# Optimization experiments

Hardware: AMD Instinct MI355X
Metric: run time of the kernel (lower is better)

The kernel has to match this reference:

```python
import jax, jax.numpy as jnp
import numpy as np

EPS = 1.1920929e-07  # torch.finfo(float32).eps, default for F.rms_norm


def _rms_norm(x):
    # F.rms_norm(x, (D,)) with no weight
    return x * jax.lax.rsqrt(jnp.mean(jnp.square(x), axis=-1, keepdims=True) + EPS)


def setup_inputs() -> dict:
    key = jax.random.key(0)
    ks = jax.random.split(key, 10)
    B, T, V, C, NB = 4, 4096, 512, 512, 64
    s = 0.02
    return {
        "x": jax.random.normal(ks[0], (B, T, V), dtype=jnp.float32),
        "basis": jax.random.normal(ks[1], (V, 2 * NB), dtype=jnp.float32),
        # AssociativeMemoryStep params
        "q_coeffs": jax.random.normal(ks[2], (C, 2 * NB), dtype=jnp.float32) * s,
        "k_coeffs": jax.random.normal(ks[3], (C, 2 * NB), dtype=jnp.float32) * s,
        "v_coeffs": jax.random.normal(ks[4], (C, 2 * NB), dtype=jnp.float32) * s,
        "o_coeffs": jax.random.normal(ks[5], (C, 2 * NB), dtype=jnp.float32) * s,
        "decay_logit": jnp.float32(3.0),
        "mem_out_scale": jnp.float32(0.1),
        # FourierRegisterOp params
        "read_coeffs": jax.random.normal(ks[6], (C, 2 * NB), dtype=jnp.float32) * s,
        "write_coeffs": jax.random.normal(ks[7], (C, 2 * NB), dtype=jnp.float32) * s,
        "channel_mix": jax.random.normal(ks[8], (C, C), dtype=jnp.float32) * s,
        "bias": jnp.zeros((C,), dtype=jnp.float32),
        "op_out_scale": jnp.float32(0.1),
        # RegisterStep scales
        "mem_scale": jnp.ones((1,), dtype=jnp.float32),
        "op_scale": jnp.ones((1,), dtype=jnp.float32),
    }


def reference(x, basis, q_coeffs, k_coeffs, v_coeffs, o_coeffs, decay_logit,
              mem_out_scale, read_coeffs, write_coeffs, channel_mix, bias,
              op_out_scale, mem_scale, op_scale):
    B, T, V = x.shape
    dt = x.dtype

    # ---- AssociativeMemoryStep on rms_norm(x) ----
    xn = _rms_norm(x)
    q_w = basis @ q_coeffs.T  # [V, C]
    k_w = basis @ k_coeffs.T
    v_w = basis @ v_coeffs.T
    o_w = basis @ o_coeffs.T
    q = xn @ q_w  # [B, T, C]
    k = xn @ k_w
    v = xn @ v_w
    scores = jnp.einsum('btc,bsc->bts', q, k)  # [B, T, T]
    decay = jax.nn.sigmoid(decay_logit)
    pos = jnp.arange(T)
    diff = pos[None, :] - pos[:, None]  # diff[t, s] = s - t
    expn = jnp.maximum(diff - 1, 0).astype(dt)
    decay_w = jnp.power(decay.astype(dt), expn) * (diff > 0).astype(dt)  # [T, T]
    retrieved = jnp.einsum('bts,bsc->btc', scores * decay_w[None], v)
    mem_out = (retrieved @ o_w.T) * mem_out_scale.astype(dt)  # [B, T, V]
    x = x + mem_scale.astype(dt) * mem_out

    # ---- FourierRegisterOp on rms_norm(x) ----
    xn2 = _rms_norm(x)
    read_w = jax.nn.softmax(basis @ read_coeffs.T, axis=0).astype(dt)  # [V, C]
    vals = xn2 @ read_w @ channel_mix.astype(dt) + bias.astype(dt)  # [B, T, C]
    vals = jax.nn.gelu(vals, approximate=False)  # torch F.gelu default = exact
    write_w = (basis @ write_coeffs.T).astype(dt)  # [V, C]
    op_out = (vals @ write_w.T) * op_out_scale.astype(dt)  # [B, T, V]
    return x + op_scale.astype(dt) * op_out
```

## Files before the change

kernel.cpp:

```cpp
#include <hip/hip_runtime.h>
#include <math.h>

typedef __attribute__((ext_vector_type(8))) short bvec8;
typedef __attribute__((ext_vector_type(4))) short bvec4;
typedef __attribute__((ext_vector_type(4))) float fvec4;
typedef unsigned short u16;

#define MROWS 16384
#define TLEN  4096
#define DD    512
#define SWB   256
#define NT128 32
#define EPS_RMS 1.1920929e-07f

#define M_SCORE  1
#define M_RETRES 2
#define M_RSGELU 3
#define M_BRES   4

__device__ __forceinline__ u16 f2bf(float f) {
  unsigned int u = __float_as_uint(f);
  u = (u + 0x7fffu + ((u >> 16) & 1u)) >> 16;
  return (u16)u;
}
__device__ __forceinline__ float bf2f(u16 u) {
  return __uint_as_float(((unsigned int)u) << 16);
}

__device__ __forceinline__ float wred_sum(float v) {
#pragma unroll
  for (int off = 32; off > 0; off >>= 1) v += __shfl_xor(v, off, 64);
  return v;
}
__device__ __forceinline__ float wred_max(float v) {
#pragma unroll
  for (int off = 32; off > 0; off >>= 1) v = fmaxf(v, __shfl_xor(v, off, 64));
  return v;
}

__device__ __forceinline__ int xcd_swz(int bid, int chunk) {
  return (bid & 7) * chunk + (bid >> 3);
}

#define GL16(g, l) __builtin_amdgcn_global_load_lds((const __attribute__((address_space(1))) unsigned int*)(g), (__attribute__((address_space(3))) unsigned int*)(l), 16, 0, 0)

__device__ __forceinline__ void gcore(
    const u16* __restrict__ Ab, int lda,
    const u16* __restrict__ Bb, int ldb,
    u16* lds, int NT, fvec4 (*acc)[4])
{
  const int tid = threadIdx.x, lane = tid & 63, w = tid >> 6;
  const int r = lane & 15, kg = lane >> 4;
  const int wn = (w & 1) * 64;
  const int ahalf = w >> 1;
  const int ar = tid >> 3, as = (tid & 7) ^ (ar & 7);
  const int br = tid >> 2, bs = (tid & 3) ^ (br & 3);
  const u16* a0r0 = Ab + (size_t)ar * lda + as * 8;
  const u16* a0r1 = a0r0 + (size_t)32 * lda;
  const u16* a1r0 = a0r0 + (size_t)64 * lda;
  const u16* a1r1 = a0r0 + (size_t)96 * lda;
  const u16* b0r0 = Bb + (size_t)br * ldb + bs * 8;
  const u16* b0r1 = b0r0 + (size_t)64 * ldb;
  u16* ldsw = lds + w * 512;

  bvec8 af[2], bfr[4];
#define ST_A0(kt,p) { GL16(a0r0+(kt)*64, ldsw+(p)*16384+0);     GL16(a0r1+(kt)*64, ldsw+(p)*16384+2048); }
#define ST_A1(kt,p) { GL16(a1r0+(kt)*64, ldsw+(p)*16384+4096);  GL16(a1r1+(kt)*64, ldsw+(p)*16384+6144); }
#define ST_B0(kt,p) { GL16(b0r0+(kt)*64, ldsw+(p)*16384+8192);  GL16(b0r1+(kt)*64, ldsw+(p)*16384+10240); }
#define ST_B1(kt,p) { GL16(b0r0+(kt)*64+32, ldsw+(p)*16384+12288); GL16(b0r1+(kt)*64+32, ldsw+(p)*16384+14336); }
#define RD_A(mq,ks,p) { const u16* Ac = lds + (p)*16384 + ahalf*4096; \
  af[0] = *(const bvec8*)&Ac[((((mq)*2+0)*16+r)*64) + ((((ks)*4+kg)^(r&7)))*8]; \
  af[1] = *(const bvec8*)&Ac[((((mq)*2+1)*16+r)*64) + ((((ks)*4+kg)^(r&7)))*8]; }
#define RD_B(ks,p) { const u16* Bc = lds + (p)*16384 + 8192 + (ks)*4096; \
  _Pragma("unroll") for (int ni=0;ni<4;++ni) bfr[ni] = *(const bvec8*)&Bc[((wn+ni*16+r)*32) + ((kg^(r&3)))*8]; }
#define MM(mq) { __builtin_amdgcn_s_setprio(1); \
  _Pragma("unroll") for (int i=0;i<2;++i) _Pragma("unroll") for (int ni=0;ni<4;++ni) \
  acc[(mq)*2+i][ni] = __builtin_amdgcn_mfma_f32_16x16x32_bf16(af[i], bfr[ni], acc[(mq)*2+i][ni], 0,0,0); \
  __builtin_amdgcn_s_setprio(0); }

  ST_A0(0,0); ST_A1(0,0); ST_B0(0,0); ST_B1(0,0);
  ST_B0(1,1);
  asm volatile("s_waitcnt vmcnt(2)" ::: "memory");
  __builtin_amdgcn_s_barrier();
  asm volatile("" ::: "memory");
  int cur = 0;
  for (int j = 0; j < NT - 1; ++j) {
    int nx = cur ^ 1, kt = j + 1;
    ST_B1(kt,nx); ST_A0(kt,nx); ST_A1(kt,nx);
    RD_A(0,0,cur); RD_B(0,cur); MM(0);
    RD_A(1,0,cur); MM(1);
    asm volatile("s_waitcnt lgkmcnt(0)" ::: "memory");
    __builtin_amdgcn_s_barrier();
    asm volatile("" ::: "memory");
    if (j + 2 < NT) { ST_B0(j+2,cur); }
    RD_A(0,1,cur); RD_B(1,cur); MM(0);
    RD_A(1,1,cur); MM(1);
    if (j + 2 < NT) {
      asm volatile("s_waitcnt vmcnt(2) lgkmcnt(0)" ::: "memory");
    } else {
      asm volatile("s_waitcnt vmcnt(0) lgkmcnt(0)" ::: "memory");
    }
    __builtin_amdgcn_s_barrier();
    asm volatile("" ::: "memory");
    cur = nx;
  }
  RD_A(0,0,cur); RD_B(0,cur); MM(0);
  RD_A(1,0,cur); MM(1);
  RD_A(0,1,cur); RD_B(1,cur); MM(0);
  RD_A(1,1,cur); MM(1);
#undef ST_A0
#undef ST_A1
#undef ST_B0
#undef ST_B1
#undef RD_A
#undef RD_B
#undef MM
}

__global__ __launch_bounds__(256, 2) void qkv256_kernel(
    const u16* __restrict__ xb, const u16* __restrict__ qkw,
    const u16* __restrict__ wvoT,
    u16* __restrict__ qb, u16* __restrict__ kb, u16* __restrict__ voT)
{
  __shared__ __align__(16) u16 As[8192];
  __shared__ __align__(16) u16 Bs[16384];
  int tid = threadIdx.x, lane = tid & 63, w = tid >> 6;
  int r = lane & 15, kg = lane >> 4;
  int wm = (w >> 1) * 64, wn = (w & 1) * 128;

  int nb = xcd_swz(blockIdx.x, 96);
  const u16 *Ab, *Bb;
  size_t om, on;
  int vmode = 0;
  if (nb < 512) {
    Ab = xb + (size_t)(nb >> 2) * 128 * 512;
    Bb = qkw + (size_t)(nb & 3) * 256 * 512;
    om = (size_t)(nb >> 2) * 128; on = (size_t)(nb & 3) * 256;
  } else {
    vmode = 1;
    int i = nb - 512;
    Ab = wvoT + (size_t)(i >> 6) * 128 * 512;
    Bb = xb + (size_t)(i & 63) * 256 * 512;
    om = (size_t)(i >> 6) * 128; on = (size_t)(i & 63) * 256;
  }

  const u16* ap = Ab + (size_t)(tid >> 3) * 512 + (((tid & 7) ^ ((tid >> 3) & 7)) * 8);
  const u16* bp = Bb + (size_t)(tid >> 3) * 512 + (((tid & 7) ^ ((tid >> 3) & 7)) * 8);

  fvec4 acc[4][8] = {};
  for (int kt = 0; kt < 8; ++kt) {
    __builtin_amdgcn_s_barrier();
    asm volatile("" ::: "memory");
#pragma unroll
    for (int l = 0; l < 4; ++l)
      GL16(ap + (size_t)(32 * l) * 512 + kt * 64, As + w * 512 + l * 2048);
#pragma unroll
    for (int l = 0; l < 8; ++l)
      GL16(bp + (size_t)(32 * l) * 512 + kt * 64, Bs + w * 512 + l * 2048);
    asm volatile("s_waitcnt vmcnt(0)" ::: "memory");
    __builtin_amdgcn_s_barrier();
    asm volatile("" ::: "memory");
    bvec8 af[4], bf[8];
#pragma unroll
    for (int ks = 0; ks < 2; ++ks) {
#pragma unroll
      for (int mi = 0; mi < 4; ++mi) {
        int rw = wm + mi * 16 + r;
        af[mi] = *(const bvec8*)&As[rw * 64 + ((ks * 4 + kg) ^ (rw & 7)) * 8];
      }
#pragma unroll
      for (int ni = 0; ni < 8; ++ni) {
        int rw = wn + ni * 16 + r;
        bf[ni] = *(const bvec8*)&Bs[rw * 64 + ((ks * 4 + kg) ^ (rw & 7)) * 8];
      }
      __builtin_amdgcn_s_setprio(1);
#pragma unroll
      for (int mi = 0; mi < 4; ++mi)
#pragma unroll
        for (int ni = 0; ni < 8; ++ni)
          acc[mi][ni] = __builtin_amdgcn_mfma_f32_16x16x32_bf16(af[mi], bf[ni], acc[mi][ni], 0, 0, 0);
      __builtin_amdgcn_s_setprio(0);
    }
  }

  int l15 = lane & 15, lr4 = (lane >> 4) << 2;
#pragma unroll
  for (int mi = 0; mi < 4; ++mi)
#pragma unroll
    for (int ni = 0; ni < 8; ++ni)
#pragma unroll
      for (int j = 0; j < 4; ++j) {
        size_t rr = om + wm + mi * 16 + lr4 + j;
        size_t c = on + wn + ni * 16 + l15;
        float v = acc[mi][ni][j];
        if (vmode == 0) {
          u16* o = (c < 512) ? qb : kb;
          o[rr * 512 + (c & 511)] = f2bf(v);
        } else {
          voT[rr * (size_t)MROWS + c] = f2bf(v);
        }
      }
}

__global__ __launch_bounds__(256) void conv7_kernel(
    const float* __restrict__ basis, const float* __restrict__ qc, const float* __restrict__ kc,
    const float* __restrict__ vc, const float* __restrict__ oc, const float* __restrict__ rc,
    const float* __restrict__ wc,
    u16* __restrict__ basisb, u16* __restrict__ qcb, u16* __restrict__ kcb,
    u16* __restrict__ vcb, u16* __restrict__ ocb, u16* __restrict__ rcb,
    u16* __restrict__ wcb)
{
  const float* src; u16* dst;
  switch (blockIdx.y) {
    case 0: src = basis; dst = basisb; break;
    case 1: src = qc; dst = qcb; break;
    case 2: src = kc; dst = kcb; break;
    case 3: src = vc; dst = vcb; break;
    case 4: src = oc; dst = ocb; break;
    case 5: src = rc; dst = rcb; break;
    default: src = wc; dst = wcb; break;
  }
  int idx = blockIdx.x * 256 + threadIdx.x;
  float4 v = ((const float4*)src)[idx];
  union { bvec4 s; u16 u[4]; } o;
  o.u[0] = f2bf(v.x); o.u[1] = f2bf(v.y); o.u[2] = f2bf(v.z); o.u[3] = f2bf(v.w);
  ((bvec4*)dst)[idx] = o.s;
}

__global__ __launch_bounds__(256, 2) void wgen_kernel(
    const u16* __restrict__ basisb, const u16* __restrict__ qcb,
    const u16* __restrict__ kcb, const u16* __restrict__ vcb,
    const u16* __restrict__ ocb, const u16* __restrict__ wcb,
    const u16* __restrict__ rcb,
    u16* __restrict__ qwT, u16* __restrict__ kwT,
    u16* __restrict__ vwB, u16* __restrict__ owB,
    u16* __restrict__ wrB, float* __restrict__ readLog)
{
  __shared__ __align__(16) u16 lds[32768];
  int tid = threadIdx.x, lane = tid & 63, wave = tid >> 6;
  int wm = (wave >> 1) * 64, wn = (wave & 1) * 64;
  int z = blockIdx.z;
  const u16 *Az, *Bz;
  switch (z) {
    case 0: Az = qcb;    Bz = basisb; break;
    case 1: Az = kcb;    Bz = basisb; break;
    case 2: Az = basisb; Bz = vcb;    break;
    case 3: Az = basisb; Bz = ocb;    break;
    case 4: Az = basisb; Bz = wcb;    break;
    default: Az = rcb;   Bz = basisb; break;
  }
  fvec4 acc[4][4] = {};
  gcore(Az + (size_t)blockIdx.y * 128 * 128, 128,
        Bz + (size_t)blockIdx.x * 128 * 128, 128,
        lds, 2, acc);
  int l15 = lane & 15, lr4 = (lane >> 4) << 2;
  int om = blockIdx.y * 128, on = blockIdx.x * 128;
  u16* oz = (z == 0) ? qwT : (z == 1) ? kwT : (z == 2) ? vwB : (z == 3) ? owB : wrB;
#pragma unroll
  for (int mi = 0; mi < 4; ++mi)
#pragma unroll
    for (int ni = 0; ni < 4; ++ni)
#pragma unroll
      for (int j = 0; j < 4; ++j) {
        int rr = om + wm + mi * 16 + lr4 + j;
        int c = on + wn + ni * 16 + l15;
        float v = acc[mi][ni][j];
        if (z == 5) readLog[(size_t)rr * DD + c] = v;
        else        oz[(size_t)rr * DD + c] = f2bf(v);
      }
}

__global__ __launch_bounds__(256, 2) void wsmall_kernel(
    const u16* __restrict__ owB, const u16* __restrict__ vwB,
    const u16* __restrict__ mtB, const u16* __restrict__ rdV,
    u16* __restrict__ wvoT, u16* __restrict__ wrmT)
{
  __shared__ __align__(16) u16 lds[32768];
  int tid = threadIdx.x, lane = tid & 63, wave = tid >> 6;
  int wm = (wave >> 1) * 64, wn = (wave & 1) * 64;
  int z = blockIdx.z;
  const u16* A = (z == 0) ? owB : mtB;
  const u16* B = (z == 0) ? vwB : rdV;
  u16* O = (z == 0) ? wvoT : wrmT;
  fvec4 acc[4][4] = {};
  gcore(A + (size_t)blockIdx.y * 128 * 512, 512,
        B + (size_t)blockIdx.x * 128 * 512, 512,
        lds, 8, acc);
  int l15 = lane & 15, lr4 = (lane >> 4) << 2;
  int om = blockIdx.y * 128, on = blockIdx.x * 128;
#pragma unroll
  for (int mi = 0; mi < 4; ++mi)
#pragma unroll
    for (int ni = 0; ni < 4; ++ni)
#pragma unroll
      for (int j = 0; j < 4; ++j)
        O[(size_t)(om + wm + mi * 16 + lr4 + j) * DD + on + wn + ni * 16 + l15] =
            f2bf(acc[mi][ni][j]);
}

__global__ __launch_bounds__(256) void xbconv_kernel(const float* __restrict__ x,
                                                     u16* __restrict__ xb)
{
  int row = blockIdx.x * 4 + (threadIdx.x >> 6);
  int lane = threadIdx.x & 63;
  const float4* p = (const float4*)(x + (size_t)row * DD);
  float4 a = p[lane * 2], b = p[lane * 2 + 1];
  float ss = a.x*a.x + a.y*a.y + a.z*a.z + a.w*a.w
           + b.x*b.x + b.y*b.y + b.z*b.z + b.w*b.w;
  ss = wred_sum(ss);
  float rs = rsqrtf(ss * (1.f / 512.f) + EPS_RMS);
  union { bvec8 s; u16 u[8]; } o;
  o.u[0]=f2bf(a.x*rs); o.u[1]=f2bf(a.y*rs); o.u[2]=f2bf(a.z*rs); o.u[3]=f2bf(a.w*rs);
  o.u[4]=f2bf(b.x*rs); o.u[5]=f2bf(b.y*rs); o.u[6]=f2bf(b.z*rs); o.u[7]=f2bf(b.w*rs);
  *(bvec8*)&xb[(size_t)row * DD + lane * 8] = o.s;
}

__global__ __launch_bounds__(256) void smx_kernel(const float* __restrict__ logit,
                                                  u16* __restrict__ outb,
                                                  u16* __restrict__ rdV,
                                                  const float* __restrict__ mix,
                                                  u16* __restrict__ mt)
{
  int bid = blockIdx.x;
  if (bid < 128) {
    int row = bid * 4 + (threadIdx.x >> 6);
    int lane = threadIdx.x & 63;
    const float4* p = (const float4*)(logit + (size_t)row * DD);
    float4 a = p[lane * 2], b = p[lane * 2 + 1];
    float m = fmaxf(fmaxf(fmaxf(a.x, a.y), fmaxf(a.z, a.w)),
                    fmaxf(fmaxf(b.x, b.y), fmaxf(b.z, b.w)));
    m = wred_max(m);
    float e0=expf(a.x-m), e1=expf(a.y-m), e2=expf(a.z-m), e3=expf(a.w-m);
    float e4=expf(b.x-m), e5=expf(b.y-m), e6=expf(b.z-m), e7=expf(b.w-m);
    float s = wred_sum(e0+e1+e2+e3+e4+e5+e6+e7);
    float inv = 1.f / s;
    union { bvec8 sv; u16 u[8]; } o;
    o.u[0]=f2bf(e0*inv); o.u[1]=f2bf(e1*inv); o.u[2]=f2bf(e2*inv); o.u[3]=f2bf(e3*inv);
    o.u[4]=f2bf(e4*inv); o.u[5]=f2bf(e5*inv); o.u[6]=f2bf(e6*inv); o.u[7]=f2bf(e7*inv);
    *(bvec8*)&outb[(size_t)row * DD + lane * 8] = o.sv;
#pragma unroll
    for (int e = 0; e < 8; ++e)
      rdV[(size_t)(lane * 8 + e) * DD + row] = o.u[e];
  } else {
    int idx = (bid - 128) * 256 + threadIdx.x;
    int n = idx & 511, k = idx >> 9;
    mt[(size_t)n * DD + k] = f2bf(mix[idx]);
  }
}

template<int MODE>
__global__ __launch_bounds__(256, 2) void mfma1d(
    const u16* __restrict__ A, int lda,
    const u16* __restrict__ B, int ldb,
    void* outp, void* out2, int ldo,
    const float* __restrict__ resid, const u16* __restrict__ residb,
    const float* __restrict__ bias,
    const float* __restrict__ s0, const float* __restrict__ s1,
    const float* __restrict__ dlog, float* __restrict__ ssq,
    const float* __restrict__ rsv, int NT)
{
  __shared__ __align__(16) u16 lds[32768];
  int tid = threadIdx.x, lane = tid & 63, wave = tid >> 6;
  int wm = (wave >> 1) * 64, wn = (wave & 1) * 64;

  const u16 *Ab, *Bb;
  size_t om, on;
  int bxx = 0, byy = 0, bzz = 0;
  int ldoR = ldo;

  if constexpr (MODE == M_SCORE) {
    int nb = xcd_swz(blockIdx.x, 32);
    bxx = nb & 1; int rr = nb >> 1; byy = rr & 31; bzz = rr >> 5;
    Ab = A + (size_t)(bzz * TLEN + byy * 128) * lda;
    Bb = B + (size_t)(bzz * TLEN + (byy + bxx) * 128) * ldb;
    om = (size_t)(bzz * NT128 + byy) * 128; on = (size_t)bxx * 128;
  } else if constexpr (MODE == M_RETRES) {
    int nb = xcd_swz(blockIdx.x, 64);
    bxx = nb & 3; int rr = nb >> 2; byy = rr & 31; bzz = rr >> 5;
    Ab = A + (size_t)((bzz * NT128 + byy) * 128) * lda;
    Bb = B + (size_t)(bxx * 128) * ldb + (size_t)(bzz * TLEN + byy * 128);
    om = (size_t)(bzz * TLEN + byy * 128); on = (size_t)bxx * 128;
  } else {
    int nb = xcd_swz(blockIdx.x, 64);
    bxx = nb & 3; byy = nb >> 2;
    Ab = A + (size_t)(byy * 128) * lda;
    Bb = B + (size_t)(bxx * 128) * ldb;
    om = (size_t)byy * 128; on = (size_t)bxx * 128;
  }

  fvec4 acc[4][4] = {};
  gcore(Ab, lda, Bb, ldb, lds, NT, acc);

  int l15 = lane & 15, lr4 = (lane >> 4) << 2;
  float dlw = 0.f;
  if constexpr (MODE == M_SCORE) {
    float dl = *dlog;
    float dc = 1.f / (1.f + expf(-dl));
    dlw = log2f(dc);
  }
  float alpha = 1.f;
  if constexpr (MODE == M_RETRES || MODE == M_BRES) alpha = s0[0] * s1[0];

  float ss[4][4] = {};

#pragma unroll
  for (int mi = 0; mi < 4; ++mi) {
#pragma unroll
    for (int ni = 0; ni < 4; ++ni) {
#pragma unroll
      for (int j = 0; j < 4; ++j) {
        int rl = wm + mi * 16 + lr4 + j;
        int cl = wn + ni * 16 + l15;
        float v = acc[mi][ni][j];
        size_t r = om + rl, c = on + cl;
        if constexpr (MODE == M_SCORE) {
          int d = bxx * 128 + (int)cl - rl;
          int sidx = (byy + bxx) * 128 + (int)cl;
          float w2 = (d >= 1 && sidx < TLEN) ? exp2f((float)(d - 1) * dlw) : 0.f;
          ((u16*)outp)[r * (size_t)ldoR + c] = f2bf(v * w2);
        } else if constexpr (MODE == M_RETRES) {
          size_t o = r * (size_t)ldoR + c;
          float t = resid[o] + alpha * v;
          ((u16*)out2)[o] = f2bf(t);
          ss[mi][j] += t * t;
        } else if constexpr (MODE == M_BRES) {
          size_t o = r * (size_t)ldoR + c;
          ((float*)outp)[o] = bf2f(residb[o]) + alpha * v;
        } else {
          float rs_ = rsqrtf(rsv[r] * (1.f / 512.f) + EPS_RMS);
          float t = v * rs_ + bias[c];
          float g = 0.5f * t * (1.f + erff(t * 0.70710678118654752f));
          ((u16*)outp)[r * (size_t)ldoR + c] = f2bf(g);
        }
      }
    }
  }

  if constexpr (MODE == M_RETRES) {
#pragma unroll
    for (int mi = 0; mi < 4; ++mi)
#pragma unroll
      for (int j = 0; j < 4; ++j) {
        float s = ss[mi][j];
        s += __shfl_xor(s, 1, 64);
        s += __shfl_xor(s, 2, 64);
        s += __shfl_xor(s, 4, 64);
        s += __shfl_xor(s, 8, 64);
        if (l15 == 0) atomicAdd(&ssq[om + wm + mi * 16 + lr4 + j], s);
      }
  }
}

extern "C" void kernel_launch(void* const* d_in, const int* in_sizes, int n_in,
                              void* d_out, int out_size, void* d_ws, size_t ws_size,
                              hipStream_t stream) {
  const float* x       = (const float*)d_in[0];
  const float* basis   = (const float*)d_in[1];
  const float* qc      = (const float*)d_in[2];
  const float* kc      = (const float*)d_in[3];
  const float* vc      = (const float*)d_in[4];
  const float* oc      = (const float*)d_in[5];
  const float* decay_l = (const float*)d_in[6];
  const float* mos     = (const float*)d_in[7];
  const float* rc      = (const float*)d_in[8];
  const float* wc      = (const float*)d_in[9];
  const float* mix     = (const float*)d_in[10];
  const float* bias    = (const float*)d_in[11];
  const float* oos     = (const float*)d_in[12];
  const float* msc     = (const float*)d_in[13];
  const float* osc     = (const float*)d_in[14];
  float* out = (float*)d_out;

  char* w = (char*)d_ws;
  u16* basisb = (u16*)w; w += 65536 * 2;
  u16* qcb    = (u16*)w; w += 65536 * 2;
  u16* kcb    = (u16*)w; w += 65536 * 2;
  u16* vcb    = (u16*)w; w += 65536 * 2;
  u16* ocb    = (u16*)w; w += 65536 * 2;
  u16* rcb    = (u16*)w; w += 65536 * 2;
  u16* wcb    = (u16*)w; w += 65536 * 2;
  u16* qwT = (u16*)w; w += 262144 * 2;
  u16* kwT = (u16*)w; w += 262144 * 2;
  u16* vwB = (u16*)w; w += 262144 * 2;
  u16* owB = (u16*)w; w += 262144 * 2;
  u16* rdB = (u16*)w; w += 262144 * 2;
  u16* wrB = (u16*)w; w += 262144 * 2;
  u16* mtB = (u16*)w; w += 262144 * 2;
  u16* rdV = (u16*)w; w += 262144 * 2;
  u16* wvoT = (u16*)w; w += 262144 * 2;
  u16* wrmT = (u16*)w; w += 262144 * 2;
  float* readLog = (float*)w; w += 262144 * 4;
  float* ssq = (float*)w; w += 16384 * 4;
  u16* xb = (u16*)w; w += (size_t)MROWS * DD * 2;
  u16* qb = (u16*)w; w += (size_t)MROWS * DD * 2;
  u16* kb = (u16*)w; w += (size_t)(MROWS + 640) * DD * 2;
  u16* voT = (u16*)w; w += ((size_t)DD * MROWS + 2048) * 2;
  u16* sc = (u16*)w; w += (size_t)MROWS * SWB * 2;

  hipMemsetAsync(ssq, 0, 16384 * sizeof(float), stream);
  conv7_kernel<<<dim3(64, 7), 256, 0, stream>>>(basis, qc, kc, vc, oc, rc, wc,
                                                basisb, qcb, kcb, vcb, ocb, rcb, wcb);
  wgen_kernel<<<dim3(4, 4, 6), 256, 0, stream>>>(basisb, qcb, kcb, vcb, ocb, wcb, rcb,
                                                 qwT, kwT, vwB, owB, wrB, readLog);
  smx_kernel<<<1152, 256, 0, stream>>>(readLog, rdB, rdV, mix, mtB);
  wsmall_kernel<<<dim3(4, 4, 2), 256, 0, stream>>>(owB, vwB, mtB, rdV, wvoT, wrmT);
  xbconv_kernel<<<4096, 256, 0, stream>>>(x, xb);
  qkv256_kernel<<<768, 256, 0, stream>>>(xb, qwT, wvoT, qb, kb, voT);
  mfma1d<M_SCORE><<<256, 256, 0, stream>>>(qb, DD, kb, DD, sc, nullptr, SWB,
                                           nullptr, nullptr, nullptr, nullptr, nullptr, decay_l, nullptr, nullptr, 8);
  mfma1d<M_RETRES><<<512, 256, 0, stream>>>(sc, SWB, voT, MROWS, nullptr, xb, DD,
                                            x, nullptr, nullptr, msc, mos, nullptr, ssq, nullptr, 4);
  mfma1d<M_RSGELU><<<512, 256, 0, stream>>>(xb, DD, wrmT, DD, kb, nullptr, DD,
                                            nullptr, nullptr, bias, nullptr, nullptr, nullptr, nullptr, ssq, 8);
  mfma1d<M_BRES><<<512, 256, 0, stream>>>(kb, DD, wrB, DD, out, nullptr, DD,
                                          nullptr, xb, nullptr, osc, oos, nullptr, nullptr, nullptr, 8);
}
```

Before: 140.4 us.

## Fold query and key weights into one QK^T matrix to skip key projection

Scores are q·k = xn Wq Wk^T xn^T, so the combined matrix Wq Wk^T is precomputed in the small weight kernel. The score GEMM then reads xb directly in place of a separate key buffer. The QKV projection kernel drops from 768 to 512 blocks because it no longer computes keys. This removes a large activation GEMM and its writes, at the cost of one extra small weight GEMM and an extra bf16 rounding of the combined weight.

```diff
diff --git a/kernel.cpp b/kernel.cpp
--- a/kernel.cpp
+++ b/kernel.cpp
@@ -118,9 +118,9 @@
 }
 
 __global__ __launch_bounds__(256, 2) void qkv256_kernel(
-    const u16* __restrict__ xb, const u16* __restrict__ qkw,
+    const u16* __restrict__ xb, const u16* __restrict__ wqkT,
     const u16* __restrict__ wvoT,
-    u16* __restrict__ qb, u16* __restrict__ kb, u16* __restrict__ voT)
+    u16* __restrict__ qb, u16* __restrict__ voT)
 {
   __shared__ __align__(16) u16 As[8192];
   __shared__ __align__(16) u16 Bs[16384];
@@ -128,17 +128,17 @@
   int r = lane & 15, kg = lane >> 4;
   int wm = (w >> 1) * 64, wn = (w & 1) * 128;
 
-  int nb = xcd_swz(blockIdx.x, 96);
+  int nb = xcd_swz(blockIdx.x, 64);
   const u16 *Ab, *Bb;
   size_t om, on;
   int vmode = 0;
-  if (nb < 512) {
-    Ab = xb + (size_t)(nb >> 2) * 128 * 512;
-    Bb = qkw + (size_t)(nb & 3) * 256 * 512;
-    om = (size_t)(nb >> 2) * 128; on = (size_t)(nb & 3) * 256;
+  if (nb < 256) {
+    Ab = xb + (size_t)(nb >> 1) * 128 * 512;
+    Bb = wqkT + (size_t)(nb & 1) * 256 * 512;
+    om = (size_t)(nb >> 1) * 128; on = (size_t)(nb & 1) * 256;
   } else {
     vmode = 1;
-    int i = nb - 512;
+    int i = nb - 256;
     Ab = wvoT + (size_t)(i >> 6) * 128 * 512;
     Bb = xb + (size_t)(i & 63) * 256 * 512;
     om = (size_t)(i >> 6) * 128; on = (size_t)(i & 63) * 256;
@@ -194,8 +194,7 @@
         size_t c = on + wn + ni * 16 + l15;
         float v = acc[mi][ni][j];
         if (vmode == 0) {
-          u16* o = (c < 512) ? qb : kb;
-          o[rr * 512 + (c & 511)] = f2bf(v);
+          qb[rr * 512 + c] = f2bf(v);
         } else {
           voT[rr * (size_t)MROWS + c] = f2bf(v);
         }
@@ -232,7 +231,7 @@
     const u16* __restrict__ kcb, const u16* __restrict__ vcb,
     const u16* __restrict__ ocb, const u16* __restrict__ wcb,
     const u16* __restrict__ rcb,
-    u16* __restrict__ qwT, u16* __restrict__ kwT,
+    u16* __restrict__ qwB, u16* __restrict__ kwB,
     u16* __restrict__ vwB, u16* __restrict__ owB,
     u16* __restrict__ wrB, float* __restrict__ readLog)
 {
@@ -242,8 +241,8 @@
   int z = blockIdx.z;
   const u16 *Az, *Bz;
   switch (z) {
-    case 0: Az = qcb;    Bz = basisb; break;
-    case 1: Az = kcb;    Bz = basisb; break;
+    case 0: Az = basisb; Bz = qcb;    break;
+    case 1: Az = basisb; Bz = kcb;    break;
     case 2: Az = basisb; Bz = vcb;    break;
     case 3: Az = basisb; Bz = ocb;    break;
     case 4: Az = basisb; Bz = wcb;    break;
@@ -255,7 +254,7 @@
         lds, 2, acc);
   int l15 = lane & 15, lr4 = (lane >> 4) << 2;
   int om = blockIdx.y * 128, on = blockIdx.x * 128;
-  u16* oz = (z == 0) ? qwT : (z == 1) ? kwT : (z == 2) ? vwB : (z == 3) ? owB : wrB;
+  u16* oz = (z == 0) ? qwB : (z == 1) ? kwB : (z == 2) ? vwB : (z == 3) ? owB : wrB;
 #pragma unroll
   for (int mi = 0; mi < 4; ++mi)
 #pragma unroll
@@ -273,15 +272,16 @@
 __global__ __launch_bounds__(256, 2) void wsmall_kernel(
     const u16* __restrict__ owB, const u16* __restrict__ vwB,
     const u16* __restrict__ mtB, const u16* __restrict__ rdV,
-    u16* __restrict__ wvoT, u16* __restrict__ wrmT)
+    const u16* __restrict__ kwB, const u16* __restrict__ qwB,
+    u16* __restrict__ wvoT, u16* __restrict__ wrmT, u16* __restrict__ wqkT)
 {
   __shared__ __align__(16) u16 lds[32768];
   int tid = threadIdx.x, lane = tid & 63, wave = tid >> 6;
   int wm = (wave >> 1) * 64, wn = (wave & 1) * 64;
   int z = blockIdx.z;
-  const u16* A = (z == 0) ? owB : mtB;
-  const u16* B = (z == 0) ? vwB : rdV;
-  u16* O = (z == 0) ? wvoT : wrmT;
+  const u16* A = (z == 0) ? owB : (z == 1) ? mtB : kwB;
+  const u16* B = (z == 0) ? vwB : (z == 1) ? rdV : qwB;
+  u16* O = (z == 0) ? wvoT : (z == 1) ? wrmT : wqkT;
   fvec4 acc[4][4] = {};
   gcore(A + (size_t)blockIdx.y * 128 * 512, 512,
         B + (size_t)blockIdx.x * 128 * 512, 512,
@@ -479,8 +479,8 @@
   u16* ocb    = (u16*)w; w += 65536 * 2;
   u16* rcb    = (u16*)w; w += 65536 * 2;
   u16* wcb    = (u16*)w; w += 65536 * 2;
-  u16* qwT = (u16*)w; w += 262144 * 2;
-  u16* kwT = (u16*)w; w += 262144 * 2;
+  u16* qwB = (u16*)w; w += 262144 * 2;
+  u16* kwB = (u16*)w; w += 262144 * 2;
   u16* vwB = (u16*)w; w += 262144 * 2;
   u16* owB = (u16*)w; w += 262144 * 2;
   u16* rdB = (u16*)w; w += 262144 * 2;
@@ -489,11 +489,12 @@
   u16* rdV = (u16*)w; w += 262144 * 2;
   u16* wvoT = (u16*)w; w += 262144 * 2;
   u16* wrmT = (u16*)w; w += 262144 * 2;
+  u16* wqkT = (u16*)w; w += 262144 * 2;
   float* readLog = (float*)w; w += 262144 * 4;
   float* ssq = (float*)w; w += 16384 * 4;
-  u16* xb = (u16*)w; w += (size_t)MROWS * DD * 2;
+  u16* xb = (u16*)w; w += (size_t)(MROWS + 640) * DD * 2;
   u16* qb = (u16*)w; w += (size_t)MROWS * DD * 2;
-  u16* kb = (u16*)w; w += (size_t)(MROWS + 640) * DD * 2;
+  u16* kb = (u16*)w; w += (size_t)MROWS * DD * 2;
   u16* voT = (u16*)w; w += ((size_t)DD * MROWS + 2048) * 2;
   u16* sc = (u16*)w; w += (size_t)MROWS * SWB * 2;
 
@@ -501,12 +502,13 @@
   conv7_kernel<<<dim3(64, 7), 256, 0, stream>>>(basis, qc, kc, vc, oc, rc, wc,
                                                 basisb, qcb, kcb, vcb, ocb, rcb, wcb);
   wgen_kernel<<<dim3(4, 4, 6), 256, 0, stream>>>(basisb, qcb, kcb, vcb, ocb, wcb, rcb,
-                                                 qwT, kwT, vwB, owB, wrB, readLog);
+                                                 qwB, kwB, vwB, owB, wrB, readLog);
   smx_kernel<<<1152, 256, 0, stream>>>(readLog, rdB, rdV, mix, mtB);
-  wsmall_kernel<<<dim3(4, 4, 2), 256, 0, stream>>>(owB, vwB, mtB, rdV, wvoT, wrmT);
+  wsmall_kernel<<<dim3(4, 4, 3), 256, 0, stream>>>(owB, vwB, mtB, rdV, kwB, qwB,
+                                                   wvoT, wrmT, wqkT);
   xbconv_kernel<<<4096, 256, 0, stream>>>(x, xb);
-  qkv256_kernel<<<768, 256, 0, stream>>>(xb, qwT, wvoT, qb, kb, voT);
-  mfma1d<M_SCORE><<<256, 256, 0, stream>>>(qb, DD, kb, DD, sc, nullptr, SWB,
+  qkv256_kernel<<<512, 256, 0, stream>>>(xb, wqkT, wvoT, qb, voT);
+  mfma1d<M_SCORE><<<256, 256, 0, stream>>>(qb, DD, xb, DD, sc, nullptr, SWB,
                                            nullptr, nullptr, nullptr, nullptr, nullptr, decay_l, nullptr, nullptr, 8);
   mfma1d<M_RETRES><<<512, 256, 0, stream>>>(sc, SWB, voT, MROWS, nullptr, xb, DD,
                                             x, nullptr, nullptr, msc, mos, nullptr, ssq, nullptr, 4);
```

Result: faster. 129.9 us (-7.5%).
